# Kernel tuning notes

Hardware: AMD Instinct MI355X
Metric: run time of the kernel (lower is better)

## Reference

```python
import jax, jax.numpy as jnp
import numpy as np

F = 64      # input_v_size
E = 64      # emb_v_size
H = 8       # int(sqrt(emb_v_size))
P = 512     # proj_e_size
B, T = 64, 256


def setup_inputs() -> dict:
    key = jax.random.key(0)
    ks = jax.random.split(key, 14)
    s1 = 1.0            # Linear(1->H): fan_in=1
    s2 = 1.0 / np.sqrt(H)
    s3 = 1.0 / np.sqrt(F * E)
    return {
        "x":    jax.random.normal(ks[0], (B, T, F), dtype=jnp.float32),
        "time": jax.random.uniform(ks[1], (B, T, F), dtype=jnp.float32),
        # stacked per-feature Linear(1->H): weight [F,H], bias [F,H]
        "w1v": jax.random.uniform(ks[2], (F, H), jnp.float32, -s1, s1),
        "b1v": jax.random.uniform(ks[3], (F, H), jnp.float32, -s1, s1),
        # stacked per-feature Linear(H->E, bias=False): [F,H,E]
        "w2v": jax.random.uniform(ks[4], (F, H, E), jnp.float32, -s2, s2),
        "w1t": jax.random.uniform(ks[5], (F, H), jnp.float32, -s1, s1),
        "b1t": jax.random.uniform(ks[6], (F, H), jnp.float32, -s1, s1),
        "w2t": jax.random.uniform(ks[7], (F, H, E), jnp.float32, -s2, s2),
        # Wx, Wt: Linear(F*E -> P) stored as [F*E, P] (= torch weight.T)
        "wx":  jax.random.uniform(ks[8], (F * E, P), jnp.float32, -s3, s3),
        "bx":  jax.random.uniform(ks[9], (P,), jnp.float32, -s3, s3),
        "wt":  jax.random.uniform(ks[10], (F * E, P), jnp.float32, -s3, s3),
        "bt":  jax.random.uniform(ks[11], (P,), jnp.float32, -s3, s3),
    }


def _branch(inp, w1, b1, w2):
    # inp [B,T,F]; w1,b1 [F,H]; w2 [F,H,E]
    h = jnp.tanh(inp[..., None] * w1 + b1)          # [B,T,F,H]
    e = jnp.einsum("btfh,fhe->btfe", h, w2)          # [B,T,F,E]
    return e.reshape(*inp.shape[:2], -1)              # [B,T,F*E]


def reference(x, time, w1v, b1v, w2v, w1t, b1t, w2t, wx, bx, wt, bt):
    x_out = _branch(x, w1v, b1v, w2v)
    t_out = _branch(time, w1t, b1t, w2t)
    return (x_out @ wx + bx) + (t_out @ wt + bt)      # [B,T,P]
```

## Files before the change

### kernel.cpp

```cpp
#include <hip/hip_runtime.h>
#include <cstdint>
#include <cstddef>

#define FF 64
#define EE 64
#define HH 8
#define PP 512
#define MM 16384
#define KK 1024

typedef __bf16 bf16x8 __attribute__((ext_vector_type(8)));
typedef float  floatx4 __attribute__((ext_vector_type(4)));

__device__ __forceinline__ unsigned short f2bf(float f) {
    unsigned int u = __float_as_uint(f);
    u += 0x7FFFu + ((u >> 16) & 1u);
    return (unsigned short)(u >> 16);
}

__device__ __forceinline__ unsigned pack2(unsigned short a, unsigned short b) {
    return (unsigned)a | ((unsigned)b << 16);
}

__device__ __forceinline__ float fast_tanh_s(float t) {
    float e, r;
    asm("v_exp_f32 %0, %1" : "=v"(e) : "v"(t));
    float d = e + 1.0f;
    asm("v_rcp_f32 %0, %1" : "=v"(r) : "v"(d));
    return __builtin_fmaf(-2.0f, r, 1.0f);
}

__device__ __forceinline__ void gl_lds16(const unsigned short* g, unsigned short* s) {
    __builtin_amdgcn_global_load_lds(
        (__attribute__((address_space(1))) void*)(void*)g,
        (__attribute__((address_space(3))) void*)s,
        16, 0, 0);
}

__global__ __launch_bounds__(256) void combine_kernel(
    const float* __restrict__ w2v, const float* __restrict__ w2t,
    const float* __restrict__ wx,  const float* __restrict__ wt,
    unsigned short* __restrict__ BmatT)
{
    const int tid = threadIdx.x;
    const int bid = blockIdx.x;
    const int br = bid >> 7;
    const int f  = (bid >> 1) & 63;
    const int nh = bid & 1;
    const float* __restrict__ w2 = br ? w2t : w2v;
    const float* __restrict__ W  = br ? wt  : wx;
    __shared__ float w2s[HH * EE];
    for (int i = tid; i < HH * EE; i += 256) w2s[i] = w2[f * HH * EE + i];
    __syncthreads();
    const int n = nh * 256 + tid;
    float acc[HH] = {0,0,0,0,0,0,0,0};
    const float* Wcol = W + (size_t)f * EE * PP + n;
    #pragma unroll 8
    for (int e = 0; e < EE; ++e) {
        const float wv = Wcol[(size_t)e * PP];
        #pragma unroll
        for (int h = 0; h < HH; ++h)
            acc[h] = __builtin_fmaf(w2s[h * EE + e], wv, acc[h]);
    }
    uint4 v;
    v.x = pack2(f2bf(acc[0]), f2bf(acc[1]));
    v.y = pack2(f2bf(acc[2]), f2bf(acc[3]));
    v.z = pack2(f2bf(acc[4]), f2bf(acc[5]));
    v.w = pack2(f2bf(acc[6]), f2bf(acc[7]));
    *reinterpret_cast<uint4*>(&BmatT[(size_t)n * KK + br * 512 + f * 8]) = v;
}

__global__ __launch_bounds__(512, 4) void gemm_fused_kernel(
    const float* __restrict__ x,   const float* __restrict__ tmv,
    const float* __restrict__ w1v, const float* __restrict__ b1v,
    const float* __restrict__ w1t, const float* __restrict__ b1t,
    const unsigned short* __restrict__ Bt,
    const float* __restrict__ bx, const float* __restrict__ bt,
    float* __restrict__ out)
{
    __shared__ __align__(16) unsigned short As[64 * 64];
    __shared__ __align__(16) unsigned short Bs[256 * 64];
    __shared__ __align__(16) float w1s[2 * FF * HH];
    __shared__ __align__(16) float b1s[2 * FF * HH];

    const int tid  = threadIdx.x;
    const int wave = tid >> 6;
    const int lane = tid & 63;
    const int m0 = blockIdx.x * 64;
    const int n0 = blockIdx.y * 256;

    {
        const float c = 2.8853900817779268f;
        #pragma unroll
        for (int t = 0; t < 2; ++t) {
            const int idx = tid + t * 512;
            const int br  = idx >> 9;
            const int rem = idx & 511;
            w1s[idx] = (br ? w1t : w1v)[rem] * c;
            b1s[idx] = (br ? b1t : b1v)[rem] * c;
        }
    }
    __syncthreads();

    const int wm  = wave >> 2;
    const int wn  = wave & 3;
    const int q   = lane >> 4;
    const int ml  = lane & 15;
    const int mlx = ml & 7;
    const int lr  = lane >> 3;
    const int lkg = ((lane & 7) ^ lr) * 8;
    const int fi  = tid & 7;
    const int arow = tid >> 3;
    const int pchunk = (fi ^ (arow & 7)) * 8;

    floatx4 acc[2][4];
    #pragma unroll
    for (int i = 0; i < 2; ++i)
        #pragma unroll
        for (int j = 0; j < 4; ++j)
            acc[i][j] = (floatx4){0.f, 0.f, 0.f, 0.f};

    for (int k0 = 0; k0 < KK; k0 += 64) {
        const int br = k0 >> 9;
        const int f0 = (k0 >> 3) & 63;

        #pragma unroll
        for (int i = 0; i < 4; ++i) {
            const int seg = wave * 4 + i;
            gl_lds16(&Bt[(size_t)(n0 + seg * 8 + lr) * KK + k0 + lkg], &Bs[seg * 512]);
        }

        {
            const float* __restrict__ inp = br ? tmv : x;
            const int f = f0 + fi;
            const float val = inp[(size_t)(m0 + arow) * FF + f];
            const float4 wlo = reinterpret_cast<const float4*>(w1s)[br * 128 + f * 2];
            const float4 whi = reinterpret_cast<const float4*>(w1s)[br * 128 + f * 2 + 1];
            const float4 blo = reinterpret_cast<const float4*>(b1s)[br * 128 + f * 2];
            const float4 bhi = reinterpret_cast<const float4*>(b1s)[br * 128 + f * 2 + 1];
            float hv[8];
            hv[0] = fast_tanh_s(__builtin_fmaf(val, wlo.x, blo.x));
            hv[1] = fast_tanh_s(__builtin_fmaf(val, wlo.y, blo.y));
            hv[2] = fast_tanh_s(__builtin_fmaf(val, wlo.z, blo.z));
            hv[3] = fast_tanh_s(__builtin_fmaf(val, wlo.w, blo.w));
            hv[4] = fast_tanh_s(__builtin_fmaf(val, whi.x, bhi.x));
            hv[5] = fast_tanh_s(__builtin_fmaf(val, whi.y, bhi.y));
            hv[6] = fast_tanh_s(__builtin_fmaf(val, whi.z, bhi.z));
            hv[7] = fast_tanh_s(__builtin_fmaf(val, whi.w, bhi.w));
            uint4 v;
            v.x = pack2(f2bf(hv[0]), f2bf(hv[1]));
            v.y = pack2(f2bf(hv[2]), f2bf(hv[3]));
            v.z = pack2(f2bf(hv[4]), f2bf(hv[5]));
            v.w = pack2(f2bf(hv[6]), f2bf(hv[7]));
            *reinterpret_cast<uint4*>(&As[arow * 64 + pchunk]) = v;
        }
        __syncthreads();

        #pragma unroll
        for (int kk = 0; kk < 64; kk += 32) {
            const int cl = (kk >> 3) + q;
            const int co = (cl ^ mlx) * 8;
            bf16x8 af[2], bfr[4];
            #pragma unroll
            for (int mt = 0; mt < 2; ++mt)
                af[mt] = *reinterpret_cast<const bf16x8*>(
                    &As[(wm * 32 + mt * 16 + ml) * 64 + co]);
            #pragma unroll
            for (int nt = 0; nt < 4; ++nt)
                bfr[nt] = *reinterpret_cast<const bf16x8*>(
                    &Bs[(wn * 64 + nt * 16 + ml) * 64 + co]);
            #pragma unroll
            for (int mt = 0; mt < 2; ++mt)
                #pragma unroll
                for (int nt = 0; nt < 4; ++nt)
                    acc[mt][nt] = __builtin_amdgcn_mfma_f32_16x16x32_bf16(
                        af[mt], bfr[nt], acc[mt][nt], 0, 0, 0);
        }
        __syncthreads();
    }

    float bias[4];
    #pragma unroll
    for (int nt = 0; nt < 4; ++nt) {
        const int n = n0 + wn * 64 + nt * 16 + ml;
        bias[nt] = bx[n] + bt[n];
    }
    #pragma unroll
    for (int mt = 0; mt < 2; ++mt) {
        const int mb = m0 + wm * 32 + mt * 16 + q * 4;
        #pragma unroll
        for (int r = 0; r < 4; ++r) {
            float* orow = out + (size_t)(mb + r) * PP + n0 + wn * 64 + ml;
            #pragma unroll
            for (int nt = 0; nt < 4; ++nt)
                orow[nt * 16] = acc[mt][nt][r] + bias[nt];
        }
    }
}

extern "C" void kernel_launch(void* const* d_in, const int* in_sizes, int n_in,
                              void* d_out, int out_size, void* d_ws, size_t ws_size,
                              hipStream_t stream)
{
    const float* x   = (const float*)d_in[0];
    const float* tmv = (const float*)d_in[1];
    const float* w1v = (const float*)d_in[2];
    const float* b1v = (const float*)d_in[3];
    const float* w2v = (const float*)d_in[4];
    const float* w1t = (const float*)d_in[5];
    const float* b1t = (const float*)d_in[6];
    const float* w2t = (const float*)d_in[7];
    const float* wx  = (const float*)d_in[8];
    const float* bx  = (const float*)d_in[9];
    const float* wt  = (const float*)d_in[10];
    const float* bt  = (const float*)d_in[11];
    float* out = (float*)d_out;

    unsigned short* Bws = (unsigned short*)d_ws;

    combine_kernel<<<256, 256, 0, stream>>>(w2v, w2t, wx, wt, Bws);
    gemm_fused_kernel<<<dim3(MM / 64, PP / 256), 512, 0, stream>>>(
        x, tmv, w1v, b1v, w1t, b1t, Bws, bx, bt, out);
}
```

Before: 125.3 us.

## Double-buffer LDS tiles and enlarge M tile to 128 in fused GEMM

The fused tanh-embedding GEMM now uses a 128x256 block tile with double-buffered A and B shared-memory tiles. The next K-step's B loads and input reads are issued before the current MFMAs, and the tanh A-tile for the next step is computed afterward, leaving one barrier per iteration. The aim is to hide global-load latency and halve B-tile reloads per output row. In exchange, LDS and register use roughly double, occupancy bounds drop to 2 blocks per CU, and the grid shrinks to 256 blocks.

```diff
diff --git a/kernel.cpp b/kernel.cpp
--- a/kernel.cpp
+++ b/kernel.cpp
@@ -8,6 +8,8 @@
 #define PP 512
 #define MM 16384
 #define KK 1024
+#define BM 128
+#define BN 256
 
 typedef __bf16 bf16x8 __attribute__((ext_vector_type(8)));
 typedef float  floatx4 __attribute__((ext_vector_type(4)));
@@ -70,7 +72,7 @@
     *reinterpret_cast<uint4*>(&BmatT[(size_t)n * KK + br * 512 + f * 8]) = v;
 }
 
-__global__ __launch_bounds__(512, 4) void gemm_fused_kernel(
+__global__ __launch_bounds__(512, 2) void gemm_fused_kernel(
     const float* __restrict__ x,   const float* __restrict__ tmv,
     const float* __restrict__ w1v, const float* __restrict__ b1v,
     const float* __restrict__ w1t, const float* __restrict__ b1t,
@@ -78,16 +80,16 @@
     const float* __restrict__ bx, const float* __restrict__ bt,
     float* __restrict__ out)
 {
-    __shared__ __align__(16) unsigned short As[64 * 64];
-    __shared__ __align__(16) unsigned short Bs[256 * 64];
+    __shared__ __align__(16) unsigned short As[2][BM * 64];
+    __shared__ __align__(16) unsigned short Bs[2][BN * 64];
     __shared__ __align__(16) float w1s[2 * FF * HH];
     __shared__ __align__(16) float b1s[2 * FF * HH];
 
     const int tid  = threadIdx.x;
     const int wave = tid >> 6;
     const int lane = tid & 63;
-    const int m0 = blockIdx.x * 64;
-    const int n0 = blockIdx.y * 256;
+    const int m0 = blockIdx.x * BM;
+    const int n0 = blockIdx.y * BN;
 
     {
         const float c = 2.8853900817779268f;
@@ -113,68 +115,95 @@
     const int arow = tid >> 3;
     const int pchunk = (fi ^ (arow & 7)) * 8;
 
-    floatx4 acc[2][4];
+    floatx4 acc[4][4];
     #pragma unroll
-    for (int i = 0; i < 2; ++i)
+    for (int i = 0; i < 4; ++i)
         #pragma unroll
         for (int j = 0; j < 4; ++j)
             acc[i][j] = (floatx4){0.f, 0.f, 0.f, 0.f};
 
-    for (int k0 = 0; k0 < KK; k0 += 64) {
-        const int br = k0 >> 9;
-        const int f0 = (k0 >> 3) & 63;
-
-        #pragma unroll
-        for (int i = 0; i < 4; ++i) {
-            const int seg = wave * 4 + i;
-            gl_lds16(&Bt[(size_t)(n0 + seg * 8 + lr) * KK + k0 + lkg], &Bs[seg * 512]);
-        }
-
-        {
-            const float* __restrict__ inp = br ? tmv : x;
-            const int f = f0 + fi;
-            const float val = inp[(size_t)(m0 + arow) * FF + f];
-            const float4 wlo = reinterpret_cast<const float4*>(w1s)[br * 128 + f * 2];
-            const float4 whi = reinterpret_cast<const float4*>(w1s)[br * 128 + f * 2 + 1];
-            const float4 blo = reinterpret_cast<const float4*>(b1s)[br * 128 + f * 2];
-            const float4 bhi = reinterpret_cast<const float4*>(b1s)[br * 128 + f * 2 + 1];
-            float hv[8];
-            hv[0] = fast_tanh_s(__builtin_fmaf(val, wlo.x, blo.x));
-            hv[1] = fast_tanh_s(__builtin_fmaf(val, wlo.y, blo.y));
-            hv[2] = fast_tanh_s(__builtin_fmaf(val, wlo.z, blo.z));
-            hv[3] = fast_tanh_s(__builtin_fmaf(val, wlo.w, blo.w));
-            hv[4] = fast_tanh_s(__builtin_fmaf(val, whi.x, bhi.x));
-            hv[5] = fast_tanh_s(__builtin_fmaf(val, whi.y, bhi.y));
-            hv[6] = fast_tanh_s(__builtin_fmaf(val, whi.z, bhi.z));
-            hv[7] = fast_tanh_s(__builtin_fmaf(val, whi.w, bhi.w));
-            uint4 v;
-            v.x = pack2(f2bf(hv[0]), f2bf(hv[1]));
-            v.y = pack2(f2bf(hv[2]), f2bf(hv[3]));
-            v.z = pack2(f2bf(hv[4]), f2bf(hv[5]));
-            v.w = pack2(f2bf(hv[6]), f2bf(hv[7]));
-            *reinterpret_cast<uint4*>(&As[arow * 64 + pchunk]) = v;
-        }
-        __syncthreads();
+    auto computeA = [&](int buf, int br, int f, float v0, float v1) {
+        const float4 wlo = reinterpret_cast<const float4*>(w1s)[br * 128 + f * 2];
+        const float4 whi = reinterpret_cast<const float4*>(w1s)[br * 128 + f * 2 + 1];
+        const float4 blo = reinterpret_cast<const float4*>(b1s)[br * 128 + f * 2];
+        const float4 bhi = reinterpret_cast<const float4*>(b1s)[br * 128 + f * 2 + 1];
+        bf16x8 o0, o1;
+        o0[0] = (__bf16)fast_tanh_s(__builtin_fmaf(v0, wlo.x, blo.x));
+        o0[1] = (__bf16)fast_tanh_s(__builtin_fmaf(v0, wlo.y, blo.y));
+        o0[2] = (__bf16)fast_tanh_s(__builtin_fmaf(v0, wlo.z, blo.z));
+        o0[3] = (__bf16)fast_tanh_s(__builtin_fmaf(v0, wlo.w, blo.w));
+        o0[4] = (__bf16)fast_tanh_s(__builtin_fmaf(v0, whi.x, bhi.x));
+        o0[5] = (__bf16)fast_tanh_s(__builtin_fmaf(v0, whi.y, bhi.y));
+        o0[6] = (__bf16)fast_tanh_s(__builtin_fmaf(v0, whi.z, bhi.z));
+        o0[7] = (__bf16)fast_tanh_s(__builtin_fmaf(v0, whi.w, bhi.w));
+        o1[0] = (__bf16)fast_tanh_s(__builtin_fmaf(v1, wlo.x, blo.x));
+        o1[1] = (__bf16)fast_tanh_s(__builtin_fmaf(v1, wlo.y, blo.y));
+        o1[2] = (__bf16)fast_tanh_s(__builtin_fmaf(v1, wlo.z, blo.z));
+        o1[3] = (__bf16)fast_tanh_s(__builtin_fmaf(v1, wlo.w, blo.w));
+        o1[4] = (__bf16)fast_tanh_s(__builtin_fmaf(v1, whi.x, bhi.x));
+        o1[5] = (__bf16)fast_tanh_s(__builtin_fmaf(v1, whi.y, bhi.y));
+        o1[6] = (__bf16)fast_tanh_s(__builtin_fmaf(v1, whi.z, bhi.z));
+        o1[7] = (__bf16)fast_tanh_s(__builtin_fmaf(v1, whi.w, bhi.w));
+        *reinterpret_cast<bf16x8*>(&As[buf][arow * 64 + pchunk])        = o0;
+        *reinterpret_cast<bf16x8*>(&As[buf][(arow + 64) * 64 + pchunk]) = o1;
+    };
+
+    {
+        #pragma unroll
+        for (int j = 0; j < 4; ++j) {
+            const int seg = wave * 4 + j;
+            gl_lds16(&Bt[(size_t)(n0 + seg * 8 + lr) * KK + lkg], &Bs[0][seg * 512]);
+        }
+        const float v0 = x[(size_t)(m0 + arow) * FF + fi];
+        const float v1 = x[(size_t)(m0 + arow + 64) * FF + fi];
+        computeA(0, 0, fi, v0, v1);
+    }
+    __syncthreads();
+
+    #pragma unroll 2
+    for (int i = 0; i < 16; ++i) {
+        const int cur = i & 1;
+        float nv0 = 0.f, nv1 = 0.f;
+
+        if (i < 15) {
+            const int in  = i + 1;
+            const int k0n = in * 64;
+            #pragma unroll
+            for (int j = 0; j < 4; ++j) {
+                const int seg = wave * 4 + j;
+                gl_lds16(&Bt[(size_t)(n0 + seg * 8 + lr) * KK + k0n + lkg],
+                         &Bs[cur ^ 1][seg * 512]);
+            }
+            const float* __restrict__ inp = (in & 8) ? tmv : x;
+            const int fn = ((in & 7) << 3) + fi;
+            nv0 = inp[(size_t)(m0 + arow) * FF + fn];
+            nv1 = inp[(size_t)(m0 + arow + 64) * FF + fn];
+        }
 
         #pragma unroll
         for (int kk = 0; kk < 64; kk += 32) {
             const int cl = (kk >> 3) + q;
             const int co = (cl ^ mlx) * 8;
-            bf16x8 af[2], bfr[4];
-            #pragma unroll
-            for (int mt = 0; mt < 2; ++mt)
+            bf16x8 af[4], bfr[4];
+            #pragma unroll
+            for (int mt = 0; mt < 4; ++mt)
                 af[mt] = *reinterpret_cast<const bf16x8*>(
-                    &As[(wm * 32 + mt * 16 + ml) * 64 + co]);
+                    &As[cur][(wm * 64 + mt * 16 + ml) * 64 + co]);
             #pragma unroll
             for (int nt = 0; nt < 4; ++nt)
                 bfr[nt] = *reinterpret_cast<const bf16x8*>(
-                    &Bs[(wn * 64 + nt * 16 + ml) * 64 + co]);
-            #pragma unroll
-            for (int mt = 0; mt < 2; ++mt)
+                    &Bs[cur][(wn * 64 + nt * 16 + ml) * 64 + co]);
+            #pragma unroll
+            for (int mt = 0; mt < 4; ++mt)
                 #pragma unroll
                 for (int nt = 0; nt < 4; ++nt)
                     acc[mt][nt] = __builtin_amdgcn_mfma_f32_16x16x32_bf16(
                         af[mt], bfr[nt], acc[mt][nt], 0, 0, 0);
+        }
+
+        if (i < 15) {
+            const int in = i + 1;
+            computeA(cur ^ 1, in >> 3, ((in & 7) << 3) + fi, nv0, nv1);
         }
         __syncthreads();
     }
@@ -186,8 +215,8 @@
         bias[nt] = bx[n] + bt[n];
     }
     #pragma unroll
-    for (int mt = 0; mt < 2; ++mt) {
-        const int mb = m0 + wm * 32 + mt * 16 + q * 4;
+    for (int mt = 0; mt < 4; ++mt) {
+        const int mb = m0 + wm * 64 + mt * 16 + q * 4;
         #pragma unroll
         for (int r = 0; r < 4; ++r) {
             float* orow = out + (size_t)(mb + r) * PP + n0 + wn * 64 + ml;
@@ -219,6 +248,6 @@
     unsigned short* Bws = (unsigned short*)d_ws;
 
     combine_kernel<<<256, 256, 0, stream>>>(w2v, w2t, wx, wt, Bws);
-    gemm_fused_kernel<<<dim3(MM / 64, PP / 256), 512, 0, stream>>>(
+    gemm_fused_kernel<<<dim3(MM / BM, PP / BN), 512, 0, stream>>>(
         x, tmv, w1v, b1v, w1t, b1t, Bws, bx, bt, out);
 }
```

New measurement: 129.5 us. 3.4% more time.
